# Kernel optimization log

Hardware: AMD Instinct MI355X
Metric: run time of the kernel (lower is better)

## Reference

```python
import jax, jax.numpy as jnp
import numpy as np

HID = 128
N_NODES = 50000
N_EDGES = 800000
N_GRAPHS = 64
N_LAYERS = 2
BN_EPS = 1e-5


def setup_inputs() -> dict:
    key = jax.random.key(0)
    ks = jax.random.split(key, 12)
    x_idx = jax.random.randint(ks[0], (N_NODES,), 0, 19)
    edge_index = jax.random.randint(ks[1], (2, N_EDGES), 0, N_NODES)
    edge_attr = jax.random.randint(ks[2], (N_EDGES,), 0, 4)
    batch = jnp.sort(jax.random.randint(ks[3], (N_NODES,), 0, N_GRAPHS))
    s = 1.0 / np.sqrt(HID)
    node_emb = jax.random.normal(ks[4], (19, HID), jnp.float32)
    edge_emb = jax.random.normal(ks[5], (4, HID), jnp.float32)
    # stacked per-layer GINE MLP params: Linear->ReLU->Linear->ReLU->BN
    W1 = jax.random.uniform(ks[6], (N_LAYERS, HID, HID), jnp.float32, -s, s)
    b1 = jnp.zeros((N_LAYERS, HID), jnp.float32)
    W2 = jax.random.uniform(ks[7], (N_LAYERS, HID, HID), jnp.float32, -s, s)
    b2 = jnp.zeros((N_LAYERS, HID), jnp.float32)
    bn_g = jnp.ones((N_LAYERS, HID), jnp.float32)
    bn_b = jnp.zeros((N_LAYERS, HID), jnp.float32)
    return {"x_idx": x_idx, "edge_index": edge_index, "edge_attr": edge_attr,
            "batch": batch, "node_emb": node_emb, "edge_emb": edge_emb,
            "W1": W1, "b1": b1, "W2": W2, "b2": b2, "bn_g": bn_g, "bn_b": bn_b}


def _gine_layer(x, e_feat, src, dst, W1, b1, W2, b2, g, beta):
    # GINEConv (eps=0): nn(x + sum_{j->i} relu(x_j + e_ji))
    msg = jax.nn.relu(x[src] + e_feat)                       # [E, H] gather
    aggr = jax.ops.segment_sum(msg, dst, num_segments=x.shape[0])  # scatter-add
    h = x + aggr
    h = jax.nn.relu(h @ W1 + b1)
    h = jax.nn.relu(h @ W2 + b2)
    mu = h.mean(0)
    var = h.var(0)
    return g * (h - mu) * jax.lax.rsqrt(var + BN_EPS) + beta  # training-mode BN


def reference(x_idx, edge_index, edge_attr, batch, node_emb, edge_emb,
              W1, b1, W2, b2, bn_g, bn_b):
    x = node_emb[x_idx]                 # [N, H]
    e_feat = edge_emb[edge_attr]        # [E, H] (encoded once, shared by layers)
    src, dst = edge_index[0], edge_index[1]
    for l in range(N_LAYERS):
        x = _gine_layer(x, e_feat, src, dst, W1[l], b1[l], W2[l], b2[l], bn_g[l], bn_b[l])
    pooled = jax.ops.segment_sum(x, batch, num_segments=N_GRAPHS)  # global_add_pool
    return pooled
```

## Files before the change

kernel.cpp:

```cpp
#include <hip/hip_runtime.h>
#include <hip/hip_bf16.h>

#define HID 128
#define NNODES 50000
#define NEDGES 800000
#define NGRAPHS 64
#define BN_EPS 1e-5f
#define CAP 64

typedef __attribute__((ext_vector_type(8))) short short8;
typedef __attribute__((ext_vector_type(4))) float f32x4;

static __device__ __forceinline__ unsigned short f2bf(float v) {
  __hip_bfloat16 b = __float2bfloat16(v);
  return *reinterpret_cast<unsigned short*>(&b);
}
static __device__ __forceinline__ float bf2f(unsigned short u) {
  return __uint_as_float(((unsigned)u) << 16);
}
static __device__ __forceinline__ float lo16f(unsigned u) {
  return __uint_as_float(u << 16);
}
static __device__ __forceinline__ float hi16f(unsigned u) {
  return __uint_as_float(u & 0xFFFF0000u);
}

static __device__ __forceinline__ unsigned packhl(float v) {
  unsigned short h = f2bf(v);
  unsigned short l = f2bf(v - bf2f(h));
  return (unsigned)h | ((unsigned)l << 16);
}
static __device__ __forceinline__ float upk(unsigned p) {
  return __uint_as_float(p << 16) + __uint_as_float(p & 0xFFFF0000u);
}
static __device__ __forceinline__ void unpack8(uint4 wa, uint4 wb,
                                               short8& hi, short8& lo) {
  union U { unsigned u[4]; short8 s; };
  U H, L;
  unsigned w[8] = {wa.x, wa.y, wa.z, wa.w, wb.x, wb.y, wb.z, wb.w};
  #pragma unroll
  for (int t = 0; t < 4; t++) {
    unsigned a = w[2 * t], b = w[2 * t + 1];
    H.u[t] = (a & 0xFFFFu) | (b << 16);
    L.u[t] = (a >> 16) | (b & 0xFFFF0000u);
  }
  hi = H.s; lo = L.s;
}

__global__ __launch_bounds__(256) void prep_kernel(
    const int* __restrict__ x_idx, const float* __restrict__ node_emb,
    unsigned int* __restrict__ xb2, const int* __restrict__ eidx,
    const int* __restrict__ eattr, int* __restrict__ cnt,
    int* __restrict__ eout, const float* __restrict__ W1,
    const float* __restrict__ W2, unsigned short* __restrict__ Wpk) {
  int i = blockIdx.x * 256 + threadIdx.x;
  int stride = gridDim.x * 256;
  const float2* ne2 = (const float2*)node_emb;
  for (int t = i; t < NNODES * (HID / 2); t += stride) {
    int n = t >> 6;
    int c2 = t & 63;
    float2 v = ne2[x_idx[n] * 64 + c2];
    xb2[t] = (unsigned)f2bf(v.x) | ((unsigned)f2bf(v.y) << 16);
  }
  for (int e = i; e < NEDGES; e += stride) {
    int s = eidx[e];
    int d = eidx[NEDGES + e];
    int ty = x_idx[s];
    int pos = atomicAdd(&cnt[d], 1);
    if (pos < CAP)
      eout[((size_t)d << 6) + pos] = s | (eattr[e] << 16) | (ty << 18);
  }
  for (int idx = i; idx < 65536; idx += stride) {
    int j = idx & 7;
    int l = (idx >> 3) & 63;
    int q = (idx >> 9) & 3;
    int t = (idx >> 11) & 7;
    int m = idx >> 14;
    int k = ((l >> 4) << 3) + j + (q << 5);
    int n = (t << 4) + (l & 15);
    int layer = m >> 1;
    const float* W = (m & 1) ? W2 : W1;
    float w = W[(size_t)layer * HID * HID + k * HID + n];
    unsigned short h = f2bf(w);
    Wpk[idx] = h;
    Wpk[idx + 65536] = f2bf(w - bf2f(h));
  }
}

#define NT 32
#define LDAF 132
#define MROW 68
#define GRID_GINE ((NNODES + NT - 1) / NT)

template <bool L0>
__global__ __launch_bounds__(512, 4) void gine_mlp_kernel(
    const unsigned short* __restrict__ in_bf,
    const float* __restrict__ instats,
    const float* __restrict__ gam, const float* __restrict__ bet,
    const int* __restrict__ cnt, const int* __restrict__ eout,
    const float* __restrict__ node_emb, const float* __restrict__ edge_emb,
    const short8* __restrict__ Wh, const short8* __restrict__ Wl,
    const float* __restrict__ b1, const float* __restrict__ b2,
    unsigned short* __restrict__ out_bf, float* __restrict__ stats,
    const int* __restrict__ batch, float* __restrict__ gpool) {
  extern __shared__ __align__(16) char smem[];
  unsigned* hAp = (unsigned*)smem;
  float* sheL = (float*)(smem + NT * LDAF * 4);
  unsigned* msgT = (unsigned*)(smem + NT * LDAF * 4);
  float* red = (float*)(smem + NT * LDAF * 4);

  const int tid = threadIdx.x;
  const int lane = tid & 63;
  const int wave = tid >> 6;
  const int base = blockIdx.x * NT;

  float scl_lo = 1.0f, scl_hi = 1.0f, sh_lo = 0.0f, sh_hi = 0.0f;

  if constexpr (L0) {
    for (int t = tid; t < 77 * 64; t += 512) {
      int combo = t >> 6, c2 = (t & 63) << 1;
      unsigned v = 0;
      if (combo < 76) {
        int ty = combo >> 2, at = combo & 3;
        float a0 = fmaxf(node_emb[ty * HID + c2] + edge_emb[at * HID + c2], 0.f);
        float a1 = fmaxf(node_emb[ty * HID + c2 + 1] + edge_emb[at * HID + c2 + 1], 0.f);
        v = (unsigned)f2bf(a0) | ((unsigned)f2bf(a1) << 16);
      }
      msgT[combo * MROW + (t & 63)] = v;
    }
  } else {
    if (tid < 4 * HID) {
      int c = tid & 127;
      float mu = instats[c] * (1.0f / NNODES);
      float var = instats[HID + c] * (1.0f / NNODES) - mu * mu;
      float s = gam[c] * rsqrtf(var + BN_EPS);
      float shc = bet[c] - mu * s;
      sheL[tid] = shc + edge_emb[tid];
    }
    {
      int c0 = lane << 1;
      float mu0 = instats[c0] * (1.0f / NNODES);
      float var0 = instats[HID + c0] * (1.0f / NNODES) - mu0 * mu0;
      scl_lo = gam[c0] * rsqrtf(var0 + BN_EPS);
      sh_lo = bet[c0] - mu0 * scl_lo;
      float mu1 = instats[c0 + 1] * (1.0f / NNODES);
      float var1 = instats[HID + c0 + 1] * (1.0f / NNODES) - mu1 * mu1;
      scl_hi = gam[c0 + 1] * rsqrtf(var1 + BN_EPS);
      sh_hi = bet[c0 + 1] - mu1 * scl_hi;
    }
  }
  __syncthreads();

  {
    const unsigned* in4 = (const unsigned*)in_bf;
    int node0 = base + wave * 4;
    float acc0[4], acc1[4];
    #pragma unroll
    for (int i = 0; i < 4; i++) { acc0[i] = 0.0f; acc1[i] = 0.0f; }

    int dg4[4], epw4[4];
    unsigned sv4[4];
    #pragma unroll
    for (int i = 0; i < 4; i++) {
      int node = node0 + i;
      bool v = node < NNODES;
      dg4[i] = v ? __builtin_amdgcn_readfirstlane(min(cnt[node], CAP)) : 0;
      epw4[i] = v ? eout[(node << 6) + lane] : 0;
      sv4[i] = v ? in4[(node << 6) + lane] : 0u;
    }

#define GL_ISSUE(SB, X, A)                                      \
    {                                                           \
      _Pragma("unroll")                                         \
      for (int jj = 0; jj < 8; jj++) {                          \
        if ((SB) + jj < dg) {                                   \
          int w = __builtin_amdgcn_readlane(epw, (SB) + jj);    \
          A[jj] = (w >> 16) & 3;                                \
          X[jj] = in4[((w & 0xFFFF) << 6) + lane];              \
        }                                                       \
      }                                                         \
    }
#define GL_CONS(SB, X, A)                                       \
    {                                                           \
      _Pragma("unroll")                                         \
      for (int jj = 0; jj < 8; jj++) {                          \
        if ((SB) + jj < dg) {                                   \
          float e0 = sheL[(A[jj] << 7) + (lane << 1)];          \
          float e1 = sheL[(A[jj] << 7) + (lane << 1) + 1];      \
          acc0[i] += fmaxf(fmaf(lo16f(X[jj]), scl_lo, e0), 0.0f); \
          acc1[i] += fmaxf(fmaf(hi16f(X[jj]), scl_hi, e1), 0.0f); \
        }                                                       \
      }                                                         \
    }

    #pragma unroll
    for (int i = 0; i < 4; i++) {
      int node = node0 + i;
      if (node >= NNODES) continue;
      int dg = dg4[i];
      int epw = epw4[i];
      if constexpr (L0) {
        acc0[i] = lo16f(sv4[i]);
        acc1[i] = hi16f(sv4[i]);
      } else {
        acc0[i] = fmaf(lo16f(sv4[i]), scl_lo, sh_lo);
        acc1[i] = fmaf(hi16f(sv4[i]), scl_hi, sh_hi);
      }
      if constexpr (L0) {
        #pragma unroll 2
        for (int j = 0; j < dg; j++) {
          int w = __builtin_amdgcn_readlane(epw, j);
          unsigned m = msgT[(((w >> 16) & 127) * MROW) + lane];
          acc0[i] += lo16f(m);
          acc1[i] += hi16f(m);
        }
      } else {
        if (dg > 0) {
          unsigned X0[8], X1[8];
          int A0[8], A1[8];
          GL_ISSUE(0, X0, A0);
          int s = 0;
          for (;;) {
            if (s * 8 + 8 < dg) GL_ISSUE(s * 8 + 8, X1, A1);
            GL_CONS(s * 8, X0, A0);
            s++;
            if (s * 8 >= dg) break;
            if (s * 8 + 8 < dg) GL_ISSUE(s * 8 + 8, X0, A0);
            GL_CONS(s * 8, X1, A1);
            s++;
            if (s * 8 >= dg) break;
          }
        }
      }
    }
#undef GL_ISSUE
#undef GL_CONS

    #pragma unroll
    for (int i = 0; i < 4; i++) {
      int nrow = wave * 4 + i;
      hAp[nrow * LDAF + (lane << 1)] = packhl(acc0[i]);
      hAp[nrow * LDAF + (lane << 1) + 1] = packhl(acc1[i]);
    }
  }
  __syncthreads();

  const int col = lane & 15;
  const int quad = lane >> 4;
  const int rbase = quad * 4;
  const int ch0 = wave * 16 + col;
  const int aoff = quad * 8;

  {
    f32x4 a0 = {0.f, 0.f, 0.f, 0.f}, a1 = a0;
    #pragma unroll
    for (int q = 0; q < 4; q++) {
      int f0 = wave * 256 + q * 64 + lane;
      short8 b0h = Wh[f0], b0l = Wl[f0];
      const unsigned* r0 = &hAp[col * LDAF + q * 32 + aoff];
      const unsigned* r1 = &hAp[(16 + col) * LDAF + q * 32 + aoff];
      short8 a0h, a0l, a1h, a1l;
      unpack8(*(const uint4*)r0, *(const uint4*)(r0 + 4), a0h, a0l);
      unpack8(*(const uint4*)r1, *(const uint4*)(r1 + 4), a1h, a1l);
      a0 = __builtin_amdgcn_mfma_f32_16x16x32_bf16(a0h, b0h, a0, 0, 0, 0);
      a0 = __builtin_amdgcn_mfma_f32_16x16x32_bf16(a0l, b0h, a0, 0, 0, 0);
      a0 = __builtin_amdgcn_mfma_f32_16x16x32_bf16(a0h, b0l, a0, 0, 0, 0);
      a1 = __builtin_amdgcn_mfma_f32_16x16x32_bf16(a1h, b0h, a1, 0, 0, 0);
      a1 = __builtin_amdgcn_mfma_f32_16x16x32_bf16(a1l, b0h, a1, 0, 0, 0);
      a1 = __builtin_amdgcn_mfma_f32_16x16x32_bf16(a1h, b0l, a1, 0, 0, 0);
    }
    __syncthreads();
    float bb0 = b1[ch0];
    #pragma unroll
    for (int r = 0; r < 4; r++) {
      hAp[(rbase + r) * LDAF + ch0] = packhl(fmaxf(a0[r] + bb0, 0.0f));
      hAp[(16 + rbase + r) * LDAF + ch0] = packhl(fmaxf(a1[r] + bb0, 0.0f));
    }
  }
  __syncthreads();

  {
    f32x4 a0 = {0.f, 0.f, 0.f, 0.f}, a1 = a0;
    #pragma unroll
    for (int q = 0; q < 4; q++) {
      int f0 = 2048 + wave * 256 + q * 64 + lane;
      short8 b0h = Wh[f0], b0l = Wl[f0];
      const unsigned* r0 = &hAp[col * LDAF + q * 32 + aoff];
      const unsigned* r1 = &hAp[(16 + col) * LDAF + q * 32 + aoff];
      short8 a0h, a0l, a1h, a1l;
      unpack8(*(const uint4*)r0, *(const uint4*)(r0 + 4), a0h, a0l);
      unpack8(*(const uint4*)r1, *(const uint4*)(r1 + 4), a1h, a1l);
      a0 = __builtin_amdgcn_mfma_f32_16x16x32_bf16(a0h, b0h, a0, 0, 0, 0);
      a0 = __builtin_amdgcn_mfma_f32_16x16x32_bf16(a0l, b0h, a0, 0, 0, 0);
      a0 = __builtin_amdgcn_mfma_f32_16x16x32_bf16(a0h, b0l, a0, 0, 0, 0);
      a1 = __builtin_amdgcn_mfma_f32_16x16x32_bf16(a1h, b0h, a1, 0, 0, 0);
      a1 = __builtin_amdgcn_mfma_f32_16x16x32_bf16(a1l, b0h, a1, 0, 0, 0);
      a1 = __builtin_amdgcn_mfma_f32_16x16x32_bf16(a1h, b0l, a1, 0, 0, 0);
    }
    __syncthreads();
    float bb0 = b2[ch0];
    #pragma unroll
    for (int r = 0; r < 4; r++) {
      hAp[(rbase + r) * LDAF + ch0] = packhl(fmaxf(a0[r] + bb0, 0.0f));
      hAp[(16 + rbase + r) * LDAF + ch0] = packhl(fmaxf(a1[r] + bb0, 0.0f));
    }
  }
  __syncthreads();

  float lsum = 0.0f, lsq = 0.0f;
  if (tid < 256) {
    const int c = tid & 127;
    const int yy = tid >> 7;
    if (out_bf) {
      #pragma unroll 4
      for (int i = 0; i < 16; i++) {
        int n = yy * 16 + i;
        int node = base + n;
        if (node < NNODES) {
          unsigned p = hAp[n * LDAF + c];
          out_bf[node * HID + c] = (unsigned short)(p & 0xFFFF);
          float v = upk(p);
          lsum += v;
          lsq += v * v;
        }
      }
    } else {
      int curg = -1;
      float pacc = 0.0f;
      for (int i = 0; i < 16; i++) {
        int n = yy * 16 + i;
        int node = base + n;
        if (node < NNODES) {
          float v = upk(hAp[n * LDAF + c]);
          lsum += v;
          lsq += v * v;
          int bg = batch[node];
          if (bg != curg) {
            if (curg >= 0) unsafeAtomicAdd(&gpool[curg * HID + c], pacc);
            curg = bg;
            pacc = 0.0f;
          }
          pacc += v;
        }
      }
      if (curg >= 0) unsafeAtomicAdd(&gpool[curg * HID + c], pacc);
    }
    if (tid >= 128) {
      red[tid - 128] = lsum;
      red[tid] = lsq;
    }
  }
  __syncthreads();
  if (tid < 128) {
    lsum += red[tid];
    lsq += red[128 + tid];
    unsafeAtomicAdd(&stats[tid], lsum);
    unsafeAtomicAdd(&stats[HID + tid], lsq);
  }
}

__device__ __forceinline__ int lbound(const int* __restrict__ arr, int n,
                                      int key) {
  int lo = 0, hi = n;
  while (lo < hi) {
    int mid = (lo + hi) >> 1;
    if (arr[mid] < key) lo = mid + 1; else hi = mid;
  }
  return lo;
}

__global__ __launch_bounds__(128) void finish_kernel(
    const float* __restrict__ gpool, const float* __restrict__ stats,
    const float* __restrict__ gam, const float* __restrict__ bet,
    const int* __restrict__ batch, float* __restrict__ out) {
  __shared__ int cnt_s;
  int g = blockIdx.x, c = threadIdx.x;
  if (c == 0)
    cnt_s = lbound(batch, NNODES, g + 1) - lbound(batch, NNODES, g);
  __syncthreads();
  float mu = stats[c] * (1.0f / NNODES);
  float var = stats[HID + c] * (1.0f / NNODES) - mu * mu;
  float scl = gam[c] * rsqrtf(var + BN_EPS);
  float sh = bet[c] - mu * scl;
  out[g * HID + c] = fmaf(gpool[g * HID + c], scl, (float)cnt_s * sh);
}

extern "C" void kernel_launch(void* const* d_in, const int* in_sizes, int n_in,
                              void* d_out, int out_size, void* d_ws, size_t ws_size,
                              hipStream_t stream) {
  const int* x_idx = (const int*)d_in[0];
  const int* eidx = (const int*)d_in[1];
  const int* eattr = (const int*)d_in[2];
  const int* batch = (const int*)d_in[3];
  const float* node_emb = (const float*)d_in[4];
  const float* edge_emb = (const float*)d_in[5];
  const float* W1 = (const float*)d_in[6];
  const float* b1 = (const float*)d_in[7];
  const float* W2 = (const float*)d_in[8];
  const float* b2 = (const float*)d_in[9];
  const float* bn_g = (const float*)d_in[10];
  const float* bn_b = (const float*)d_in[11];
  float* out = (float*)d_out;

  const size_t nfeat = (size_t)NNODES * HID;
  unsigned short* xbf = (unsigned short*)d_ws;
  unsigned short* h2bf = xbf + nfeat;
  float* stats0 = (float*)(h2bf + nfeat);
  float* stats1 = stats0 + 2 * HID;
  float* gpool = stats1 + 2 * HID;
  int* cnt = (int*)(gpool + NGRAPHS * HID);
  int* eout = cnt + NNODES;
  unsigned short* Wpk = (unsigned short*)(eout + (size_t)NNODES * CAP);
  size_t needed = (size_t)((char*)(Wpk + 131072) - (char*)d_ws);
  if (ws_size < needed) return;

  hipMemsetAsync(stats0, 0, (4 * HID + NGRAPHS * HID + NNODES) * sizeof(int),
                 stream);

  prep_kernel<<<1024, 256, 0, stream>>>(x_idx, node_emb, (unsigned int*)xbf,
                                        eidx, eattr, cnt, eout, W1, W2, Wpk);

  const short8* Wfh = (const short8*)Wpk;
  const short8* Wfl = Wfh + 8192;
  const size_t smem0 = (size_t)NT * LDAF * 4 + 77 * MROW * 4;
  const size_t smem1 = (size_t)NT * LDAF * 4 + 4 * HID * 4;
  gine_mlp_kernel<true><<<GRID_GINE, 512, smem0, stream>>>(
      xbf, nullptr, nullptr, nullptr, cnt, eout, node_emb, edge_emb,
      Wfh + 0 * 2048, Wfl + 0 * 2048, b1, b2, h2bf, stats0, nullptr, nullptr);
  gine_mlp_kernel<false><<<GRID_GINE, 512, smem1, stream>>>(
      h2bf, stats0, bn_g, bn_b, cnt, eout, node_emb, edge_emb,
      Wfh + 2 * 2048, Wfl + 2 * 2048, b1 + HID, b2 + HID, nullptr, stats1,
      batch, gpool);
  finish_kernel<<<NGRAPHS, 128, 0, stream>>>(gpool, stats1, bn_g + HID,
                                             bn_b + HID, batch, out);
}
```

Baseline: 293.1 us.

## Use 48-node tiles, precompute layer-0 message table globally, pipeline gathers

The node tile per block grows from 32 to 48: each wave now aggregates 6 nodes and the MLP adds a third 16-row MFMA tile. The layer-0 message table (relu of node embedding plus edge embedding) is built once in the prep kernel in global memory, so each block no longer rebuilds it in shared memory. Layer-0 gathers are now issued in double-buffered batches of 8. The launch bound rises to 8 blocks per CU and shared memory shrinks. In exchange there are fewer blocks, more register pressure from the higher occupancy target, and layer-0 table reads go through cache instead of LDS.

Measured after the change: 302.4 us. 1.03x slower.

```diff
diff --git a/kernel.cpp b/kernel.cpp
--- a/kernel.cpp
+++ b/kernel.cpp
@@ -52,7 +52,8 @@
     unsigned int* __restrict__ xb2, const int* __restrict__ eidx,
     const int* __restrict__ eattr, int* __restrict__ cnt,
     int* __restrict__ eout, const float* __restrict__ W1,
-    const float* __restrict__ W2, unsigned short* __restrict__ Wpk) {
+    const float* __restrict__ W2, unsigned short* __restrict__ Wpk,
+    unsigned* __restrict__ msgTg, const float* __restrict__ edge_emb) {
   int i = blockIdx.x * 256 + threadIdx.x;
   int stride = gridDim.x * 256;
   const float2* ne2 = (const float2*)node_emb;
@@ -69,6 +70,13 @@
     int pos = atomicAdd(&cnt[d], 1);
     if (pos < CAP)
       eout[((size_t)d << 6) + pos] = s | (eattr[e] << 16) | (ty << 18);
+  }
+  for (int idx = i; idx < 76 * 64; idx += stride) {
+    int combo = idx >> 6, c2 = (idx & 63) << 1;
+    int ty = combo >> 2, at = combo & 3;
+    float a0 = fmaxf(node_emb[ty * HID + c2] + edge_emb[at * HID + c2], 0.f);
+    float a1 = fmaxf(node_emb[ty * HID + c2 + 1] + edge_emb[at * HID + c2 + 1], 0.f);
+    msgTg[idx] = (unsigned)f2bf(a0) | ((unsigned)f2bf(a1) << 16);
   }
   for (int idx = i; idx < 65536; idx += stride) {
     int j = idx & 7;
@@ -87,18 +95,17 @@
   }
 }
 
-#define NT 32
+#define NT 48
 #define LDAF 132
-#define MROW 68
 #define GRID_GINE ((NNODES + NT - 1) / NT)
 
 template <bool L0>
-__global__ __launch_bounds__(512, 4) void gine_mlp_kernel(
+__global__ __launch_bounds__(512, 8) void gine_mlp_kernel(
     const unsigned short* __restrict__ in_bf,
     const float* __restrict__ instats,
     const float* __restrict__ gam, const float* __restrict__ bet,
     const int* __restrict__ cnt, const int* __restrict__ eout,
-    const float* __restrict__ node_emb, const float* __restrict__ edge_emb,
+    const unsigned* __restrict__ msgTg, const float* __restrict__ edge_emb,
     const short8* __restrict__ Wh, const short8* __restrict__ Wl,
     const float* __restrict__ b1, const float* __restrict__ b2,
     unsigned short* __restrict__ out_bf, float* __restrict__ stats,
@@ -106,7 +113,6 @@
   extern __shared__ __align__(16) char smem[];
   unsigned* hAp = (unsigned*)smem;
   float* sheL = (float*)(smem + NT * LDAF * 4);
-  unsigned* msgT = (unsigned*)(smem + NT * LDAF * 4);
   float* red = (float*)(smem + NT * LDAF * 4);
 
   const int tid = threadIdx.x;
@@ -116,19 +122,7 @@
 
   float scl_lo = 1.0f, scl_hi = 1.0f, sh_lo = 0.0f, sh_hi = 0.0f;
 
-  if constexpr (L0) {
-    for (int t = tid; t < 77 * 64; t += 512) {
-      int combo = t >> 6, c2 = (t & 63) << 1;
-      unsigned v = 0;
-      if (combo < 76) {
-        int ty = combo >> 2, at = combo & 3;
-        float a0 = fmaxf(node_emb[ty * HID + c2] + edge_emb[at * HID + c2], 0.f);
-        float a1 = fmaxf(node_emb[ty * HID + c2 + 1] + edge_emb[at * HID + c2 + 1], 0.f);
-        v = (unsigned)f2bf(a0) | ((unsigned)f2bf(a1) << 16);
-      }
-      msgT[combo * MROW + (t & 63)] = v;
-    }
-  } else {
+  if constexpr (!L0) {
     if (tid < 4 * HID) {
       int c = tid & 127;
       float mu = instats[c] * (1.0f / NNODES);
@@ -148,25 +142,25 @@
       scl_hi = gam[c0 + 1] * rsqrtf(var1 + BN_EPS);
       sh_hi = bet[c0 + 1] - mu1 * scl_hi;
     }
-  }
-  __syncthreads();
+    __syncthreads();
+  }
 
   {
     const unsigned* in4 = (const unsigned*)in_bf;
-    int node0 = base + wave * 4;
-    float acc0[4], acc1[4];
-    #pragma unroll
-    for (int i = 0; i < 4; i++) { acc0[i] = 0.0f; acc1[i] = 0.0f; }
-
-    int dg4[4], epw4[4];
-    unsigned sv4[4];
-    #pragma unroll
-    for (int i = 0; i < 4; i++) {
+    int node0 = base + wave * 6;
+    float acc0[6], acc1[6];
+    #pragma unroll
+    for (int i = 0; i < 6; i++) { acc0[i] = 0.0f; acc1[i] = 0.0f; }
+
+    int dg6[6], epw6[6];
+    unsigned sv6[6];
+    #pragma unroll
+    for (int i = 0; i < 6; i++) {
       int node = node0 + i;
       bool v = node < NNODES;
-      dg4[i] = v ? __builtin_amdgcn_readfirstlane(min(cnt[node], CAP)) : 0;
-      epw4[i] = v ? eout[(node << 6) + lane] : 0;
-      sv4[i] = v ? in4[(node << 6) + lane] : 0u;
+      dg6[i] = v ? __builtin_amdgcn_readfirstlane(min(cnt[node], CAP)) : 0;
+      epw6[i] = v ? eout[(node << 6) + lane] : 0;
+      sv6[i] = v ? in4[(node << 6) + lane] : 0u;
     }
 
 #define GL_ISSUE(SB, X, A)                                      \
@@ -185,37 +179,62 @@
       _Pragma("unroll")                                         \
       for (int jj = 0; jj < 8; jj++) {                          \
         if ((SB) + jj < dg) {                                   \
-          float e0 = sheL[(A[jj] << 7) + (lane << 1)];          \
-          float e1 = sheL[(A[jj] << 7) + (lane << 1) + 1];      \
-          acc0[i] += fmaxf(fmaf(lo16f(X[jj]), scl_lo, e0), 0.0f); \
-          acc1[i] += fmaxf(fmaf(hi16f(X[jj]), scl_hi, e1), 0.0f); \
+          float2 e2 = *(const float2*)&sheL[(A[jj] << 7) + (lane << 1)]; \
+          acc0[i] += fmaxf(fmaf(lo16f(X[jj]), scl_lo, e2.x), 0.0f); \
+          acc1[i] += fmaxf(fmaf(hi16f(X[jj]), scl_hi, e2.y), 0.0f); \
         }                                                       \
       }                                                         \
     }
-
-    #pragma unroll
-    for (int i = 0; i < 4; i++) {
+#define GT_ISSUE(SB, M)                                         \
+    {                                                           \
+      _Pragma("unroll")                                         \
+      for (int jj = 0; jj < 8; jj++) {                          \
+        if ((SB) + jj < dg) {                                   \
+          int w = __builtin_amdgcn_readlane(epw, (SB) + jj);    \
+          M[jj] = msgTg[(((w >> 16) & 127) << 6) + lane];       \
+        }                                                       \
+      }                                                         \
+    }
+#define GT_CONS(SB, M)                                          \
+    {                                                           \
+      _Pragma("unroll")                                         \
+      for (int jj = 0; jj < 8; jj++) {                          \
+        if ((SB) + jj < dg) {                                   \
+          acc0[i] += lo16f(M[jj]);                              \
+          acc1[i] += hi16f(M[jj]);                              \
+        }                                                       \
+      }                                                         \
+    }
+
+    #pragma unroll
+    for (int i = 0; i < 6; i++) {
       int node = node0 + i;
       if (node >= NNODES) continue;
-      int dg = dg4[i];
-      int epw = epw4[i];
+      int dg = dg6[i];
+      int epw = epw6[i];
       if constexpr (L0) {
-        acc0[i] = lo16f(sv4[i]);
-        acc1[i] = hi16f(sv4[i]);
+        acc0[i] = lo16f(sv6[i]);
+        acc1[i] = hi16f(sv6[i]);
       } else {
-        acc0[i] = fmaf(lo16f(sv4[i]), scl_lo, sh_lo);
-        acc1[i] = fmaf(hi16f(sv4[i]), scl_hi, sh_hi);
+        acc0[i] = fmaf(lo16f(sv6[i]), scl_lo, sh_lo);
+        acc1[i] = fmaf(hi16f(sv6[i]), scl_hi, sh_hi);
       }
-      if constexpr (L0) {
-        #pragma unroll 2
-        for (int j = 0; j < dg; j++) {
-          int w = __builtin_amdgcn_readlane(epw, j);
-          unsigned m = msgT[(((w >> 16) & 127) * MROW) + lane];
-          acc0[i] += lo16f(m);
-          acc1[i] += hi16f(m);
-        }
-      } else {
-        if (dg > 0) {
+      if (dg > 0) {
+        if constexpr (L0) {
+          unsigned M0[8], M1[8];
+          GT_ISSUE(0, M0);
+          int s = 0;
+          for (;;) {
+            if (s * 8 + 8 < dg) GT_ISSUE(s * 8 + 8, M1);
+            GT_CONS(s * 8, M0);
+            s++;
+            if (s * 8 >= dg) break;
+            if (s * 8 + 8 < dg) GT_ISSUE(s * 8 + 8, M0);
+            GT_CONS(s * 8, M1);
+            s++;
+            if (s * 8 >= dg) break;
+          }
+        } else {
           unsigned X0[8], X1[8];
           int A0[8], A1[8];
           GL_ISSUE(0, X0, A0);
@@ -235,10 +254,12 @@
     }
 #undef GL_ISSUE
 #undef GL_CONS
-
-    #pragma unroll
-    for (int i = 0; i < 4; i++) {
-      int nrow = wave * 4 + i;
+#undef GT_ISSUE
+#undef GT_CONS
+
+    #pragma unroll
+    for (int i = 0; i < 6; i++) {
+      int nrow = wave * 6 + i;
       hAp[nrow * LDAF + (lane << 1)] = packhl(acc0[i]);
       hAp[nrow * LDAF + (lane << 1) + 1] = packhl(acc1[i]);
     }
@@ -252,22 +273,27 @@
   const int aoff = quad * 8;
 
   {
-    f32x4 a0 = {0.f, 0.f, 0.f, 0.f}, a1 = a0;
+    f32x4 a0 = {0.f, 0.f, 0.f, 0.f}, a1 = a0, a2 = a0;
     #pragma unroll
     for (int q = 0; q < 4; q++) {
       int f0 = wave * 256 + q * 64 + lane;
       short8 b0h = Wh[f0], b0l = Wl[f0];
       const unsigned* r0 = &hAp[col * LDAF + q * 32 + aoff];
       const unsigned* r1 = &hAp[(16 + col) * LDAF + q * 32 + aoff];
-      short8 a0h, a0l, a1h, a1l;
+      const unsigned* r2 = &hAp[(32 + col) * LDAF + q * 32 + aoff];
+      short8 a0h, a0l, a1h, a1l, a2h, a2l;
       unpack8(*(const uint4*)r0, *(const uint4*)(r0 + 4), a0h, a0l);
       unpack8(*(const uint4*)r1, *(const uint4*)(r1 + 4), a1h, a1l);
+      unpack8(*(const uint4*)r2, *(const uint4*)(r2 + 4), a2h, a2l);
       a0 = __builtin_amdgcn_mfma_f32_16x16x32_bf16(a0h, b0h, a0, 0, 0, 0);
       a0 = __builtin_amdgcn_mfma_f32_16x16x32_bf16(a0l, b0h, a0, 0, 0, 0);
       a0 = __builtin_amdgcn_mfma_f32_16x16x32_bf16(a0h, b0l, a0, 0, 0, 0);
       a1 = __builtin_amdgcn_mfma_f32_16x16x32_bf16(a1h, b0h, a1, 0, 0, 0);
       a1 = __builtin_amdgcn_mfma_f32_16x16x32_bf16(a1l, b0h, a1, 0, 0, 0);
       a1 = __builtin_amdgcn_mfma_f32_16x16x32_bf16(a1h, b0l, a1, 0, 0, 0);
+      a2 = __builtin_amdgcn_mfma_f32_16x16x32_bf16(a2h, b0h, a2, 0, 0, 0);
+      a2 = __builtin_amdgcn_mfma_f32_16x16x32_bf16(a2l, b0h, a2, 0, 0, 0);
+      a2 = __builtin_amdgcn_mfma_f32_16x16x32_bf16(a2h, b0l, a2, 0, 0, 0);
     }
     __syncthreads();
     float bb0 = b1[ch0];
@@ -275,27 +301,33 @@
     for (int r = 0; r < 4; r++) {
       hAp[(rbase + r) * LDAF + ch0] = packhl(fmaxf(a0[r] + bb0, 0.0f));
       hAp[(16 + rbase + r) * LDAF + ch0] = packhl(fmaxf(a1[r] + bb0, 0.0f));
+      hAp[(32 + rbase + r) * LDAF + ch0] = packhl(fmaxf(a2[r] + bb0, 0.0f));
     }
   }
   __syncthreads();
 
   {
-    f32x4 a0 = {0.f, 0.f, 0.f, 0.f}, a1 = a0;
+    f32x4 a0 = {0.f, 0.f, 0.f, 0.f}, a1 = a0, a2 = a0;
     #pragma unroll
     for (int q = 0; q < 4; q++) {
       int f0 = 2048 + wave * 256 + q * 64 + lane;
       short8 b0h = Wh[f0], b0l = Wl[f0];
       const unsigned* r0 = &hAp[col * LDAF + q * 32 + aoff];
       const unsigned* r1 = &hAp[(16 + col) * LDAF + q * 32 + aoff];
-      short8 a0h, a0l, a1h, a1l;
+      const unsigned* r2 = &hAp[(32 + col) * LDAF + q * 32 + aoff];
+      short8 a0h, a0l, a1h, a1l, a2h, a2l;
       unpack8(*(const uint4*)r0, *(const uint4*)(r0 + 4), a0h, a0l);
       unpack8(*(const uint4*)r1, *(const uint4*)(r1 + 4), a1h, a1l);
+      unpack8(*(const uint4*)r2, *(const uint4*)(r2 + 4), a2h, a2l);
       a0 = __builtin_amdgcn_mfma_f32_16x16x32_bf16(a0h, b0h, a0, 0, 0, 0);
       a0 = __builtin_amdgcn_mfma_f32_16x16x32_bf16(a0l, b0h, a0, 0, 0, 0);
       a0 = __builtin_amdgcn_mfma_f32_16x16x32_bf16(a0h, b0l, a0, 0, 0, 0);
       a1 = __builtin_amdgcn_mfma_f32_16x16x32_bf16(a1h, b0h, a1, 0, 0, 0);
       a1 = __builtin_amdgcn_mfma_f32_16x16x32_bf16(a1l, b0h, a1, 0, 0, 0);
       a1 = __builtin_amdgcn_mfma_f32_16x16x32_bf16(a1h, b0l, a1, 0, 0, 0);
+      a2 = __builtin_amdgcn_mfma_f32_16x16x32_bf16(a2h, b0h, a2, 0, 0, 0);
+      a2 = __builtin_amdgcn_mfma_f32_16x16x32_bf16(a2l, b0h, a2, 0, 0, 0);
+      a2 = __builtin_amdgcn_mfma_f32_16x16x32_bf16(a2h, b0l, a2, 0, 0, 0);
     }
     __syncthreads();
     float bb0 = b2[ch0];
@@ -303,6 +335,7 @@
     for (int r = 0; r < 4; r++) {
       hAp[(rbase + r) * LDAF + ch0] = packhl(fmaxf(a0[r] + bb0, 0.0f));
       hAp[(16 + rbase + r) * LDAF + ch0] = packhl(fmaxf(a1[r] + bb0, 0.0f));
+      hAp[(32 + rbase + r) * LDAF + ch0] = packhl(fmaxf(a2[r] + bb0, 0.0f));
     }
   }
   __syncthreads();
@@ -313,8 +346,8 @@
     const int yy = tid >> 7;
     if (out_bf) {
       #pragma unroll 4
-      for (int i = 0; i < 16; i++) {
-        int n = yy * 16 + i;
+      for (int i = 0; i < 24; i++) {
+        int n = yy * 24 + i;
         int node = base + n;
         if (node < NNODES) {
           unsigned p = hAp[n * LDAF + c];
@@ -327,8 +360,8 @@
     } else {
       int curg = -1;
       float pacc = 0.0f;
-      for (int i = 0; i < 16; i++) {
-        int n = yy * 16 + i;
+      for (int i = 0; i < 24; i++) {
+        int n = yy * 24 + i;
         int node = base + n;
         if (node < NNODES) {
           float v = upk(hAp[n * LDAF + c]);
@@ -411,24 +444,25 @@
   int* cnt = (int*)(gpool + NGRAPHS * HID);
   int* eout = cnt + NNODES;
   unsigned short* Wpk = (unsigned short*)(eout + (size_t)NNODES * CAP);
-  size_t needed = (size_t)((char*)(Wpk + 131072) - (char*)d_ws);
+  unsigned* msgTg = (unsigned*)(Wpk + 131072);
+  size_t needed = (size_t)((char*)(msgTg + 76 * 64) - (char*)d_ws);
   if (ws_size < needed) return;
 
   hipMemsetAsync(stats0, 0, (4 * HID + NGRAPHS * HID + NNODES) * sizeof(int),
                  stream);
 
   prep_kernel<<<1024, 256, 0, stream>>>(x_idx, node_emb, (unsigned int*)xbf,
-                                        eidx, eattr, cnt, eout, W1, W2, Wpk);
+                                        eidx, eattr, cnt, eout, W1, W2, Wpk,
+                                        msgTg, edge_emb);
 
   const short8* Wfh = (const short8*)Wpk;
   const short8* Wfl = Wfh + 8192;
-  const size_t smem0 = (size_t)NT * LDAF * 4 + 77 * MROW * 4;
-  const size_t smem1 = (size_t)NT * LDAF * 4 + 4 * HID * 4;
-  gine_mlp_kernel<true><<<GRID_GINE, 512, smem0, stream>>>(
-      xbf, nullptr, nullptr, nullptr, cnt, eout, node_emb, edge_emb,
+  const size_t smemsz = (size_t)NT * LDAF * 4 + 4 * HID * 4;
+  gine_mlp_kernel<true><<<GRID_GINE, 512, smemsz, stream>>>(
+      xbf, nullptr, nullptr, nullptr, cnt, eout, msgTg, edge_emb,
       Wfh + 0 * 2048, Wfl + 0 * 2048, b1, b2, h2bf, stats0, nullptr, nullptr);
-  gine_mlp_kernel<false><<<GRID_GINE, 512, smem1, stream>>>(
-      h2bf, stats0, bn_g, bn_b, cnt, eout, node_emb, edge_emb,
+  gine_mlp_kernel<false><<<GRID_GINE, 512, smemsz, stream>>>(
+      h2bf, stats0, bn_g, bn_b, cnt, eout, msgTg, edge_emb,
       Wfh + 2 * 2048, Wfl + 2 * 2048, b1 + HID, b2 + HID, nullptr, stats1,
       batch, gpool);
   finish_kernel<<<NGRAPHS, 128, 0, stream>>>(gpool, stats1, bn_g + HID,
```
